# Kernel optimization log

Measured on AMD Instinct MI355X. Metric: run time of the kernel, lower is better.

Reference implementation:

```python
import jax, jax.numpy as jnp
import numpy as np

EMB = 64
HID = 128
N_NODES = 50000
N_EDGES = 800000
N_Q = 64

def setup_inputs() -> dict:
    key = jax.random.key(0)
    ks = jax.random.split(key, 20)
    d = {}
    d['question_emb'] = jax.random.normal(ks[0], (N_Q, EMB), dtype=jnp.float32)
    d['node_embeddings'] = jax.random.normal(ks[1], (N_NODES, EMB), dtype=jnp.float32)
    d['edge_embeddings'] = jax.random.normal(ks[2], (N_EDGES, EMB), dtype=jnp.float32)
    d['edge_index'] = jax.random.randint(ks[3], (2, N_EDGES), 0, N_NODES, dtype=jnp.int32)
    d['node_batch'] = jnp.sort(jax.random.randint(ks[4], (N_NODES,), 0, N_Q, dtype=jnp.int32))
    s = 1.0 / np.sqrt(EMB)
    # projector weights (Linear emb->emb), stored as (in, out)
    d['Wq'] = jax.random.normal(ks[5], (EMB, EMB), dtype=jnp.float32) * s
    d['bq'] = jnp.zeros((EMB,), dtype=jnp.float32)
    d['We'] = jax.random.normal(ks[6], (EMB, EMB), dtype=jnp.float32) * s
    d['be'] = jnp.zeros((EMB,), dtype=jnp.float32)
    d['Wr'] = jax.random.normal(ks[7], (EMB, EMB), dtype=jnp.float32) * s
    d['br'] = jnp.zeros((EMB,), dtype=jnp.float32)
    # DenseFeatureExtractor: concat(4*EMB) -> EMB -> HID, ReLU after each
    d['W1'] = jax.random.normal(ks[8], (4 * EMB, EMB), dtype=jnp.float32) / np.sqrt(4 * EMB)
    d['b1'] = jnp.zeros((EMB,), dtype=jnp.float32)
    d['W2'] = jax.random.normal(ks[9], (EMB, HID), dtype=jnp.float32) * s
    d['b2'] = jnp.zeros((HID,), dtype=jnp.float32)
    # DeterministicHead: HID -> 1
    d['Wh'] = jax.random.normal(ks[10], (HID, 1), dtype=jnp.float32) / np.sqrt(HID)
    d['bh'] = jnp.zeros((1,), dtype=jnp.float32)
    return d


def reference(question_emb, node_embeddings, edge_embeddings, edge_index, node_batch,
              Wq, bq, We, be, Wr, br, W1, b1, W2, b2, Wh, bh):
    head_idx, tail_idx = edge_index[0], edge_index[1]
    query_ids = node_batch[head_idx]                       # [E]
    # projections (applied to the small tables, then gathered per edge)
    q_repr = question_emb @ Wq + bq                        # [Q, D]
    node_repr = node_embeddings @ We + be                  # [N, D]
    rel_repr = edge_embeddings @ Wr + br                   # [E, D]
    semantic = jnp.concatenate([
        q_repr[query_ids], node_repr[head_idx], rel_repr, node_repr[tail_idx]
    ], axis=-1)                                            # [E, 4D]
    h = jax.nn.relu(semantic @ W1 + b1)                    # [E, D]
    h = jax.nn.relu(h @ W2 + b2)                           # [E, H]
    logits = (h @ Wh + bh)[:, 0]                           # [E]
    scores = jax.nn.sigmoid(logits)
    return scores
```

## Files before the change

### kernel.cpp

```cpp
#include <hip/hip_runtime.h>

#define NNODE 50000
#define NEDGE 800000

typedef __attribute__((ext_vector_type(8))) short bf16x8;
typedef __attribute__((ext_vector_type(4))) float f32x4;

#define WB_QCB   0
#define WB_WRTB  8192
#define WB_W2TB  16384
#define WB_WEH   33024
#define WB_WET   49408
#define WB_NHB   65792
#define WB_NTB   6465792

__device__ inline ushort f2b(float x) {
    uint u = __float_as_uint(x);
    return (ushort)((u + 0x7fffu + ((u >> 16) & 1u)) >> 16);
}
__device__ inline uint pack2(float lo, float hi) {
    return (uint)f2b(lo) | ((uint)f2b(hi) << 16);
}
__device__ inline float bLo(uint u) { return __uint_as_float(u << 16); }
__device__ inline float bHi(uint u) { return __uint_as_float(u & 0xffff0000u); }

union B8U { uint4 u; bf16x8 b; };

__device__ inline void stage64(float* dst, const float* __restrict__ src, int t) {
    #pragma unroll
    for (int i = 0; i < 4; ++i) {
        int f = t + i * 256;
        *(float4*)&dst[f * 4] = *(const float4*)&src[f * 4];
    }
}

__device__ inline void gemm64(const float* sA, const float* sB, int t, float acc[4][4]) {
    const int r0 = (t >> 4) * 4, c0 = (t & 15) * 4;
    #pragma unroll
    for (int j = 0; j < 4; ++j)
        #pragma unroll
        for (int i = 0; i < 4; ++i) acc[j][i] = 0.f;
    #pragma unroll 4
    for (int k = 0; k < 64; ++k) {
        float4 b = *(const float4*)&sB[k * 64 + c0];
        float bv[4] = {b.x, b.y, b.z, b.w};
        #pragma unroll
        for (int j = 0; j < 4; ++j) {
            float a = sA[(r0 + j) * 64 + k];
            #pragma unroll
            for (int i = 0; i < 4; ++i) acc[j][i] = fmaf(a, bv[i], acc[j][i]);
        }
    }
}

__global__ __launch_bounds__(256)
void prep_small(const float* __restrict__ Q,
                const float* __restrict__ Wq, const float* __restrict__ bq,
                const float* __restrict__ We, const float* __restrict__ be,
                const float* __restrict__ Wr, const float* __restrict__ br,
                const float* __restrict__ W1, const float* __restrict__ b1,
                const float* __restrict__ W2, char* __restrict__ wsb)
{
    __shared__ float sA[4096], sB[4096], sC[4096], sBias[64];
    const int t = threadIdx.x;
    const int bid = blockIdx.x;
    const int r0 = (t >> 4) * 4, c0 = (t & 15) * 4;

    if (bid == 0) {
        stage64(sA, Wq, t); stage64(sB, W1, t);
        __syncthreads();
        float acc[4][4];
        gemm64(sA, sB, t, acc);
        #pragma unroll
        for (int j = 0; j < 4; ++j)
            *(float4*)&sC[(r0 + j) * 64 + c0] = make_float4(acc[j][0], acc[j][1], acc[j][2], acc[j][3]);
        if (t < 64) {
            float s = b1[t];
            for (int k = 0; k < 64; ++k) {
                s = fmaf(bq[k], W1[k * 64 + t], s);
                s = fmaf(be[k], W1[(64 + k) * 64 + t] + W1[(192 + k) * 64 + t], s);
                s = fmaf(br[k], W1[(128 + k) * 64 + t], s);
            }
            sBias[t] = s;
        }
        __syncthreads();
        stage64(sA, Q, t);
        __syncthreads();
        gemm64(sA, sC, t, acc);
        ushort* qcb = (ushort*)(wsb + WB_QCB);
        #pragma unroll
        for (int j = 0; j < 4; ++j) {
            ushort4 p;
            p.x = f2b(acc[j][0] + sBias[c0 + 0]);
            p.y = f2b(acc[j][1] + sBias[c0 + 1]);
            p.z = f2b(acc[j][2] + sBias[c0 + 2]);
            p.w = f2b(acc[j][3] + sBias[c0 + 3]);
            *(ushort4*)&qcb[(r0 + j) * 64 + c0] = p;
        }
    } else if (bid == 1 || bid == 2) {
        const float* w1seg = W1 + (bid == 1 ? 64 * 64 : 192 * 64);
        float* dst = (float*)(wsb + (bid == 1 ? WB_WEH : WB_WET));
        stage64(sA, We, t); stage64(sB, w1seg, t);
        __syncthreads();
        float acc[4][4];
        gemm64(sA, sB, t, acc);
        #pragma unroll
        for (int j = 0; j < 4; ++j)
            *(float4*)&dst[(r0 + j) * 64 + c0] = make_float4(acc[j][0], acc[j][1], acc[j][2], acc[j][3]);
    } else if (bid == 3) {
        stage64(sA, Wr, t); stage64(sB, W1 + 128 * 64, t);
        __syncthreads();
        float acc[4][4];
        gemm64(sA, sB, t, acc);
        ushort* wrtb = (ushort*)(wsb + WB_WRTB);
        #pragma unroll
        for (int j = 0; j < 4; ++j)
            #pragma unroll
            for (int i = 0; i < 4; ++i)
                wrtb[(c0 + i) * 64 + (r0 + j)] = f2b(acc[j][i]);
    } else {
        ushort* w2tb = (ushort*)(wsb + WB_W2TB);
        #pragma unroll
        for (int i = 0; i < 32; ++i) {
            int f = t + i * 256;
            int k = f >> 7, n = f & 127;
            w2tb[n * 64 + ((k & 15) * 4 + (k >> 4))] = f2b(W2[f]);
        }
    }
}

__global__ __launch_bounds__(256)
void prep_nodes(const float* __restrict__ Xn, const char* __restrict__ wsb_c,
                char* __restrict__ wsb)
{
    __shared__ float sXT[64 * 68];
    __shared__ float sWeh[4096], sWet[4096];
    const int t = threadIdx.x;
    const int nbase = blockIdx.x * 64;
    const float* Weh = (const float*)(wsb_c + WB_WEH);
    const float* Wet = (const float*)(wsb_c + WB_WET);
    ushort* nhb = (ushort*)(wsb + WB_NHB);
    ushort* ntb = (ushort*)(wsb + WB_NTB);

    #pragma unroll
    for (int i = 0; i < 4; ++i) {
        int f = t + i * 256;
        int n = f >> 4, s4 = (f & 15) * 4;
        int gn = nbase + n;
        float4 v = make_float4(0.f, 0.f, 0.f, 0.f);
        if (gn < NNODE) v = *(const float4*)&Xn[gn * 64 + s4];
        sXT[(s4 + 0) * 68 + n] = v.x;
        sXT[(s4 + 1) * 68 + n] = v.y;
        sXT[(s4 + 2) * 68 + n] = v.z;
        sXT[(s4 + 3) * 68 + n] = v.w;
    }
    #pragma unroll
    for (int i = 0; i < 4; ++i) {
        int f = t + i * 256;
        *(float4*)&sWeh[f * 4] = *(const float4*)&Weh[f * 4];
        *(float4*)&sWet[f * 4] = *(const float4*)&Wet[f * 4];
    }
    __syncthreads();

    const int er = (t >> 4) * 4, cc = (t & 15) * 4;
    float ah[4][4], at[4][4];
    #pragma unroll
    for (int j = 0; j < 4; ++j)
        #pragma unroll
        for (int i = 0; i < 4; ++i) { ah[j][i] = 0.f; at[j][i] = 0.f; }
    #pragma unroll 4
    for (int k = 0; k < 64; ++k) {
        float4 a  = *(const float4*)&sXT[k * 68 + er];
        float4 bh = *(const float4*)&sWeh[k * 64 + cc];
        float4 bt = *(const float4*)&sWet[k * 64 + cc];
        float av[4] = {a.x, a.y, a.z, a.w};
        #pragma unroll
        for (int j = 0; j < 4; ++j) {
            ah[j][0] = fmaf(av[j], bh.x, ah[j][0]); ah[j][1] = fmaf(av[j], bh.y, ah[j][1]);
            ah[j][2] = fmaf(av[j], bh.z, ah[j][2]); ah[j][3] = fmaf(av[j], bh.w, ah[j][3]);
            at[j][0] = fmaf(av[j], bt.x, at[j][0]); at[j][1] = fmaf(av[j], bt.y, at[j][1]);
            at[j][2] = fmaf(av[j], bt.z, at[j][2]); at[j][3] = fmaf(av[j], bt.w, at[j][3]);
        }
    }
    #pragma unroll
    for (int j = 0; j < 4; ++j) {
        int n = nbase + er + j;
        if (n < NNODE) {
            ushort4 ph, pt;
            ph.x = f2b(ah[j][0]); ph.y = f2b(ah[j][1]); ph.z = f2b(ah[j][2]); ph.w = f2b(ah[j][3]);
            pt.x = f2b(at[j][0]); pt.y = f2b(at[j][1]); pt.z = f2b(at[j][2]); pt.w = f2b(at[j][3]);
            *(ushort4*)&nhb[n * 64 + cc] = ph;
            *(ushort4*)&ntb[n * 64 + cc] = pt;
        }
    }
}

__global__ __launch_bounds__(256, 4)
void edge_kernel(const float* __restrict__ Xe,
                 const int* __restrict__ EI,
                 const int* __restrict__ NB,
                 const float* __restrict__ b2,
                 const float* __restrict__ Wh,
                 const float* __restrict__ bh,
                 const char* __restrict__ wsb,
                 float* __restrict__ out)
{
    __shared__ ushort sG[64 * 72];
    __shared__ ushort sH[64 * 72];
    __shared__ ushort sW2[128 * 72];
    __shared__ float  sB2s[128], sWhs[128];

    const int t = threadIdx.x;
    const int ebase = blockIdx.x * 64;
    const int l = t & 63, w = t >> 6;
    const int m = l & 15, qq = l >> 4, q8 = qq * 8;

    const ushort* qcb  = (const ushort*)(wsb + WB_QCB);
    const ushort* wrtb = (const ushort*)(wsb + WB_WRTB);
    const ushort* w2tb = (const ushort*)(wsb + WB_W2TB);
    const ushort* nhb  = (const ushort*)(wsb + WB_NHB);
    const ushort* ntb  = (const ushort*)(wsb + WB_NTB);

    const int eg = w * 16 + (l >> 2);
    const int qg = l & 3;
    int hd = EI[ebase + eg];
    int tl = EI[NEDGE + ebase + eg];
    int qi = NB[hd];

    const float* xrow = &Xe[(size_t)(ebase + w * 16 + m) * 64];
    float4 x0 = *(const float4*)&xrow[q8];
    float4 x1 = *(const float4*)&xrow[q8 + 4];
    float4 x2 = *(const float4*)&xrow[32 + q8];
    float4 x3 = *(const float4*)&xrow[32 + q8 + 4];

    B8U wrB[4][2];
    #pragma unroll
    for (int nt = 0; nt < 4; ++nt) {
        const ushort* row = &wrtb[(nt * 16 + m) * 64];
        wrB[nt][0].u = *(const uint4*)&row[q8];
        wrB[nt][1].u = *(const uint4*)&row[32 + q8];
    }

    #pragma unroll
    for (int i = 0; i < 4; ++i) {
        int f = t + i * 256;
        *(uint4*)&sW2[(f >> 3) * 72 + (f & 7) * 8] = *(const uint4*)&w2tb[f * 8];
    }
    if (t < 128) { sB2s[t] = b2[t]; sWhs[t] = Wh[t]; }
    float bh0 = bh[0];

    {
        float s[16];
        #pragma unroll
        for (int a = 0; a < 4; ++a) {
            int coff = a * 16 + qg * 4;
            uint2 gq = *(const uint2*)&qcb[qi * 64 + coff];
            uint2 gh = *(const uint2*)&nhb[(size_t)hd * 64 + coff];
            uint2 gt = *(const uint2*)&ntb[(size_t)tl * 64 + coff];
            s[a]      = bLo(gq.x) + bLo(gh.x) + bLo(gt.x);
            s[4 + a]  = bHi(gq.x) + bHi(gh.x) + bHi(gt.x);
            s[8 + a]  = bLo(gq.y) + bLo(gh.y) + bLo(gt.y);
            s[12 + a] = bHi(gq.y) + bHi(gh.y) + bHi(gt.y);
        }
        uint pk[8];
        #pragma unroll
        for (int wd = 0; wd < 8; ++wd) pk[wd] = pack2(s[2 * wd], s[2 * wd + 1]);
        *(uint4*)&sG[eg * 72 + qg * 16]     = make_uint4(pk[0], pk[1], pk[2], pk[3]);
        *(uint4*)&sG[eg * 72 + qg * 16 + 8] = make_uint4(pk[4], pk[5], pk[6], pk[7]);
    }

    B8U a0, a1;
    a0.u = make_uint4(pack2(x0.x, x0.y), pack2(x0.z, x0.w),
                      pack2(x1.x, x1.y), pack2(x1.z, x1.w));
    a1.u = make_uint4(pack2(x2.x, x2.y), pack2(x2.z, x2.w),
                      pack2(x3.x, x3.y), pack2(x3.z, x3.w));

    __syncthreads();

    f32x4 acc1[4];
    #pragma unroll
    for (int nt = 0; nt < 4; ++nt) {
        f32x4 c = {0.f, 0.f, 0.f, 0.f};
        c = __builtin_amdgcn_mfma_f32_16x16x32_bf16(a0.b, wrB[nt][0].b, c, 0, 0, 0);
        c = __builtin_amdgcn_mfma_f32_16x16x32_bf16(a1.b, wrB[nt][1].b, c, 0, 0, 0);
        acc1[nt] = c;
    }

    #pragma unroll
    for (int r = 0; r < 4; ++r) {
        int e = w * 16 + qq * 4 + r;
        uint2 gg = *(const uint2*)&sG[e * 72 + m * 4];
        uint lo = pack2(fmaxf(acc1[0][r] + bLo(gg.x), 0.f),
                        fmaxf(acc1[1][r] + bHi(gg.x), 0.f));
        uint hi = pack2(fmaxf(acc1[2][r] + bLo(gg.y), 0.f),
                        fmaxf(acc1[3][r] + bHi(gg.y), 0.f));
        *(uint2*)&sH[e * 72 + m * 4] = make_uint2(lo, hi);
    }

    bf16x8 A0 = *(const bf16x8*)&sH[(w * 16 + m) * 72 + q8];
    bf16x8 A1 = *(const bf16x8*)&sH[(w * 16 + m) * 72 + 32 + q8];
    float part[4] = {0.f, 0.f, 0.f, 0.f};
    #pragma unroll
    for (int nt = 0; nt < 8; ++nt) {
        bf16x8 B0 = *(const bf16x8*)&sW2[(nt * 16 + m) * 72 + q8];
        bf16x8 B1 = *(const bf16x8*)&sW2[(nt * 16 + m) * 72 + 32 + q8];
        f32x4 c = {0.f, 0.f, 0.f, 0.f};
        c = __builtin_amdgcn_mfma_f32_16x16x32_bf16(A0, B0, c, 0, 0, 0);
        c = __builtin_amdgcn_mfma_f32_16x16x32_bf16(A1, B1, c, 0, 0, 0);
        int col = nt * 16 + m;
        float b2v = sB2s[col], whv = sWhs[col];
        #pragma unroll
        for (int r = 0; r < 4; ++r)
            part[r] = fmaf(fmaxf(c[r] + b2v, 0.f), whv, part[r]);
    }
    #pragma unroll
    for (int md = 1; md < 16; md <<= 1) {
        part[0] += __shfl_xor(part[0], md, 64);
        part[1] += __shfl_xor(part[1], md, 64);
        part[2] += __shfl_xor(part[2], md, 64);
        part[3] += __shfl_xor(part[3], md, 64);
    }
    if (m == 0) {
        float4 o;
        o.x = 1.f / (1.f + __expf(-(part[0] + bh0)));
        o.y = 1.f / (1.f + __expf(-(part[1] + bh0)));
        o.z = 1.f / (1.f + __expf(-(part[2] + bh0)));
        o.w = 1.f / (1.f + __expf(-(part[3] + bh0)));
        *(float4*)&out[ebase + w * 16 + qq * 4] = o;
    }
}

extern "C" void kernel_launch(void* const* d_in, const int* in_sizes, int n_in,
                              void* d_out, int out_size, void* d_ws, size_t ws_size,
                              hipStream_t stream)
{
    const float* Q   = (const float*)d_in[0];
    const float* Xn  = (const float*)d_in[1];
    const float* Xe  = (const float*)d_in[2];
    const int*   EI  = (const int*)d_in[3];
    const int*   NB  = (const int*)d_in[4];
    const float* Wq  = (const float*)d_in[5];
    const float* bq  = (const float*)d_in[6];
    const float* We  = (const float*)d_in[7];
    const float* be  = (const float*)d_in[8];
    const float* Wr  = (const float*)d_in[9];
    const float* br  = (const float*)d_in[10];
    const float* W1  = (const float*)d_in[11];
    const float* b1  = (const float*)d_in[12];
    const float* W2  = (const float*)d_in[13];
    const float* b2  = (const float*)d_in[14];
    const float* Wh  = (const float*)d_in[15];
    const float* bh  = (const float*)d_in[16];
    float* out = (float*)d_out;
    char*  wsb = (char*)d_ws;

    prep_small<<<5, 256, 0, stream>>>(Q, Wq, bq, We, be, Wr, br, W1, b1, W2, wsb);
    prep_nodes<<<(NNODE + 63) / 64, 256, 0, stream>>>(Xn, wsb, wsb);
    edge_kernel<<<NEDGE / 64, 256, 0, stream>>>(Xe, EI, NB, b2, Wh, bh, wsb, out);
}
```

Measured before the change: 388.2 us.

## Precompute packed edge indices, swizzle W2 in LDS, reuse shared buffer, raise occupancy

A new prep stage packs each edge's head, tail and query id into an int4 in workspace, so the edge kernel does one coalesced load instead of dependent EI and NB gathers. W2 is stored in LDS with an XOR swizzle and no padding, and the hidden activations reuse the sG buffer, cutting LDS per block. Wr fragments are loaded right before use instead of held across the gather, and launch bounds go from 4 to 6 blocks per SIMD to raise occupancy. The row reduction switches from shuffles to DPP, and pack2 uses a byte permute; the cost is an extra 12.8 MB index write and read pass.

Result: slower. 408.0 us (+5.1%).

```diff
diff --git a/kernel.cpp b/kernel.cpp
--- a/kernel.cpp
+++ b/kernel.cpp
@@ -8,21 +8,35 @@
 
 #define WB_QCB   0
 #define WB_WRTB  8192
-#define WB_W2TB  16384
-#define WB_WEH   33024
-#define WB_WET   49408
-#define WB_NHB   65792
-#define WB_NTB   6465792
+#define WB_W2SB  16384
+#define WB_WEH   32768
+#define WB_WET   49152
+#define WB_NHB   65536
+#define WB_NTB   6465536
+#define WB_EIDX  12865536
 
 __device__ inline ushort f2b(float x) {
     uint u = __float_as_uint(x);
     return (ushort)((u + 0x7fffu + ((u >> 16) & 1u)) >> 16);
 }
 __device__ inline uint pack2(float lo, float hi) {
-    return (uint)f2b(lo) | ((uint)f2b(hi) << 16);
+    uint a = __float_as_uint(lo);
+    uint b = __float_as_uint(hi);
+    a += 0x7fffu + ((a >> 16) & 1u);
+    b += 0x7fffu + ((b >> 16) & 1u);
+    return __builtin_amdgcn_perm(b, a, 0x07060302);
 }
 __device__ inline float bLo(uint u) { return __uint_as_float(u << 16); }
 __device__ inline float bHi(uint u) { return __uint_as_float(u & 0xffff0000u); }
+
+__device__ inline float row16_reduce(float v) {
+    int x;
+    x = __builtin_amdgcn_mov_dpp(__float_as_int(v), 0x121, 0xf, 0xf, false); v += __int_as_float(x);
+    x = __builtin_amdgcn_mov_dpp(__float_as_int(v), 0x122, 0xf, 0xf, false); v += __int_as_float(x);
+    x = __builtin_amdgcn_mov_dpp(__float_as_int(v), 0x124, 0xf, 0xf, false); v += __int_as_float(x);
+    x = __builtin_amdgcn_mov_dpp(__float_as_int(v), 0x128, 0xf, 0xf, false); v += __int_as_float(x);
+    return v;
+}
 
 union B8U { uint4 u; bf16x8 b; };
 
@@ -54,17 +68,33 @@
 }
 
 __global__ __launch_bounds__(256)
-void prep_small(const float* __restrict__ Q,
-                const float* __restrict__ Wq, const float* __restrict__ bq,
-                const float* __restrict__ We, const float* __restrict__ be,
-                const float* __restrict__ Wr, const float* __restrict__ br,
-                const float* __restrict__ W1, const float* __restrict__ b1,
-                const float* __restrict__ W2, char* __restrict__ wsb)
+void prep_a(const float* __restrict__ Q,
+            const float* __restrict__ Wq, const float* __restrict__ bq,
+            const float* __restrict__ We, const float* __restrict__ be,
+            const float* __restrict__ Wr, const float* __restrict__ br,
+            const float* __restrict__ W1, const float* __restrict__ b1,
+            const float* __restrict__ W2,
+            const int* __restrict__ EI, const int* __restrict__ NB,
+            char* __restrict__ wsb)
 {
     __shared__ float sA[4096], sB[4096], sC[4096], sBias[64];
     const int t = threadIdx.x;
     const int bid = blockIdx.x;
     const int r0 = (t >> 4) * 4, c0 = (t & 15) * 4;
+
+    if (bid >= 5) {
+        int e0 = (bid - 5) * 1024 + t * 4;
+        if (e0 < NEDGE) {
+            int4 hds = *(const int4*)&EI[e0];
+            int4 tls = *(const int4*)&EI[NEDGE + e0];
+            int4* eidx = (int4*)(wsb + WB_EIDX);
+            eidx[e0 + 0] = make_int4(hds.x, tls.x, NB[hds.x], 0);
+            eidx[e0 + 1] = make_int4(hds.y, tls.y, NB[hds.y], 0);
+            eidx[e0 + 2] = make_int4(hds.z, tls.z, NB[hds.z], 0);
+            eidx[e0 + 3] = make_int4(hds.w, tls.w, NB[hds.w], 0);
+        }
+        return;
+    }
 
     if (bid == 0) {
         stage64(sA, Wq, t); stage64(sB, W1, t);
@@ -119,12 +149,13 @@
             for (int i = 0; i < 4; ++i)
                 wrtb[(c0 + i) * 64 + (r0 + j)] = f2b(acc[j][i]);
     } else {
-        ushort* w2tb = (ushort*)(wsb + WB_W2TB);
+        ushort* w2s = (ushort*)(wsb + WB_W2SB);
         #pragma unroll
         for (int i = 0; i < 32; ++i) {
             int f = t + i * 256;
             int k = f >> 7, n = f & 127;
-            w2tb[n * 64 + ((k & 15) * 4 + (k >> 4))] = f2b(W2[f]);
+            int p = (k & 15) * 4 + (k >> 4);
+            w2s[n * 64 + (((p >> 3) ^ (n & 7)) * 8) + (p & 7)] = f2b(W2[f]);
         }
     }
 }
@@ -195,19 +226,16 @@
     }
 }
 
-__global__ __launch_bounds__(256, 4)
+__global__ __launch_bounds__(256, 6)
 void edge_kernel(const float* __restrict__ Xe,
-                 const int* __restrict__ EI,
-                 const int* __restrict__ NB,
                  const float* __restrict__ b2,
                  const float* __restrict__ Wh,
                  const float* __restrict__ bh,
                  const char* __restrict__ wsb,
                  float* __restrict__ out)
 {
+    __shared__ ushort sW2[128 * 64];
     __shared__ ushort sG[64 * 72];
-    __shared__ ushort sH[64 * 72];
-    __shared__ ushort sW2[128 * 72];
     __shared__ float  sB2s[128], sWhs[128];
 
     const int t = threadIdx.x;
@@ -217,15 +245,14 @@
 
     const ushort* qcb  = (const ushort*)(wsb + WB_QCB);
     const ushort* wrtb = (const ushort*)(wsb + WB_WRTB);
-    const ushort* w2tb = (const ushort*)(wsb + WB_W2TB);
+    const ushort* w2s  = (const ushort*)(wsb + WB_W2SB);
     const ushort* nhb  = (const ushort*)(wsb + WB_NHB);
     const ushort* ntb  = (const ushort*)(wsb + WB_NTB);
+    const int4*   eidx = (const int4*)(wsb + WB_EIDX);
 
     const int eg = w * 16 + (l >> 2);
     const int qg = l & 3;
-    int hd = EI[ebase + eg];
-    int tl = EI[NEDGE + ebase + eg];
-    int qi = NB[hd];
+    int4 idx = eidx[ebase + eg];
 
     const float* xrow = &Xe[(size_t)(ebase + w * 16 + m) * 64];
     float4 x0 = *(const float4*)&xrow[q8];
@@ -233,23 +260,16 @@
     float4 x2 = *(const float4*)&xrow[32 + q8];
     float4 x3 = *(const float4*)&xrow[32 + q8 + 4];
 
-    B8U wrB[4][2];
-    #pragma unroll
-    for (int nt = 0; nt < 4; ++nt) {
-        const ushort* row = &wrtb[(nt * 16 + m) * 64];
-        wrB[nt][0].u = *(const uint4*)&row[q8];
-        wrB[nt][1].u = *(const uint4*)&row[32 + q8];
-    }
-
     #pragma unroll
     for (int i = 0; i < 4; ++i) {
         int f = t + i * 256;
-        *(uint4*)&sW2[(f >> 3) * 72 + (f & 7) * 8] = *(const uint4*)&w2tb[f * 8];
+        *(uint4*)&sW2[f * 8] = *(const uint4*)&w2s[f * 8];
     }
     if (t < 128) { sB2s[t] = b2[t]; sWhs[t] = Wh[t]; }
     float bh0 = bh[0];
 
     {
+        const int hd = idx.x, tl = idx.y, qi = idx.z;
         float s[16];
         #pragma unroll
         for (int a = 0; a < 4; ++a) {
@@ -280,9 +300,13 @@
     f32x4 acc1[4];
     #pragma unroll
     for (int nt = 0; nt < 4; ++nt) {
+        const ushort* row = &wrtb[(nt * 16 + m) * 64];
+        B8U b0, b1v;
+        b0.u  = *(const uint4*)&row[q8];
+        b1v.u = *(const uint4*)&row[32 + q8];
         f32x4 c = {0.f, 0.f, 0.f, 0.f};
-        c = __builtin_amdgcn_mfma_f32_16x16x32_bf16(a0.b, wrB[nt][0].b, c, 0, 0, 0);
-        c = __builtin_amdgcn_mfma_f32_16x16x32_bf16(a1.b, wrB[nt][1].b, c, 0, 0, 0);
+        c = __builtin_amdgcn_mfma_f32_16x16x32_bf16(a0.b, b0.b, c, 0, 0, 0);
+        c = __builtin_amdgcn_mfma_f32_16x16x32_bf16(a1.b, b1v.b, c, 0, 0, 0);
         acc1[nt] = c;
     }
 
@@ -294,32 +318,34 @@
                         fmaxf(acc1[1][r] + bHi(gg.x), 0.f));
         uint hi = pack2(fmaxf(acc1[2][r] + bLo(gg.y), 0.f),
                         fmaxf(acc1[3][r] + bHi(gg.y), 0.f));
-        *(uint2*)&sH[e * 72 + m * 4] = make_uint2(lo, hi);
-    }
-
-    bf16x8 A0 = *(const bf16x8*)&sH[(w * 16 + m) * 72 + q8];
-    bf16x8 A1 = *(const bf16x8*)&sH[(w * 16 + m) * 72 + 32 + q8];
+        *(uint2*)&sG[e * 72 + m * 4] = make_uint2(lo, hi);
+    }
+
+    bf16x8 A0 = *(const bf16x8*)&sG[(w * 16 + m) * 72 + q8];
+    bf16x8 A1 = *(const bf16x8*)&sG[(w * 16 + m) * 72 + 32 + q8];
+    const int o1 = (qq ^ (m & 7)) * 8;
+    const int o2 = o1 ^ 32;
     float part[4] = {0.f, 0.f, 0.f, 0.f};
     #pragma unroll
     for (int nt = 0; nt < 8; ++nt) {
-        bf16x8 B0 = *(const bf16x8*)&sW2[(nt * 16 + m) * 72 + q8];
-        bf16x8 B1 = *(const bf16x8*)&sW2[(nt * 16 + m) * 72 + 32 + q8];
+        B8U B0, B1;
+        B0.u = *(const uint4*)&sW2[nt * 1024 + m * 64 + o1];
+        B1.u = *(const uint4*)&sW2[nt * 1024 + m * 64 + o2];
         f32x4 c = {0.f, 0.f, 0.f, 0.f};
-        c = __builtin_amdgcn_mfma_f32_16x16x32_bf16(A0, B0, c, 0, 0, 0);
-        c = __builtin_amdgcn_mfma_f32_16x16x32_bf16(A1, B1, c, 0, 0, 0);
+        c = __builtin_amdgcn_mfma_f32_16x16x32_bf16(A0, B0.b, c, 0, 0, 0);
+        c = __builtin_amdgcn_mfma_f32_16x16x32_bf16(A1, B1.b, c, 0, 0, 0);
         int col = nt * 16 + m;
         float b2v = sB2s[col], whv = sWhs[col];
         #pragma unroll
         for (int r = 0; r < 4; ++r)
             part[r] = fmaf(fmaxf(c[r] + b2v, 0.f), whv, part[r]);
     }
-    #pragma unroll
-    for (int md = 1; md < 16; md <<= 1) {
-        part[0] += __shfl_xor(part[0], md, 64);
-        part[1] += __shfl_xor(part[1], md, 64);
-        part[2] += __shfl_xor(part[2], md, 64);
-        part[3] += __shfl_xor(part[3], md, 64);
-    }
+
+    part[0] = row16_reduce(part[0]);
+    part[1] = row16_reduce(part[1]);
+    part[2] = row16_reduce(part[2]);
+    part[3] = row16_reduce(part[3]);
+
     if (m == 0) {
         float4 o;
         o.x = 1.f / (1.f + __expf(-(part[0] + bh0)));
@@ -354,7 +380,8 @@
     float* out = (float*)d_out;
     char*  wsb = (char*)d_ws;
 
-    prep_small<<<5, 256, 0, stream>>>(Q, Wq, bq, We, be, Wr, br, W1, b1, W2, wsb);
+    prep_a<<<5 + (NEDGE + 1023) / 1024, 256, 0, stream>>>(
+        Q, Wq, bq, We, be, Wr, br, W1, b1, W2, EI, NB, wsb);
     prep_nodes<<<(NNODE + 63) / 64, 256, 0, stream>>>(Xn, wsb, wsb);
-    edge_kernel<<<NEDGE / 64, 256, 0, stream>>>(Xe, EI, NB, b2, Wh, bh, wsb, out);
-}
+    edge_kernel<<<NEDGE / 64, 256, 0, stream>>>(Xe, b2, Wh, bh, wsb, out);
+}
```
